# Kernel tuning notes

Measured on AMD Instinct MI355X. Metric: run time of the kernel, lower is better.

The kernel has to match this reference:

```python
import jax, jax.numpy as jnp
import numpy as np

ALPHA = 0.05  # default alpha in __call__
INV_SQRT2 = 0.7071067811865476


def setup_inputs() -> dict:
    key = jax.random.key(0)
    k1, k2 = jax.random.split(key)
    n_objects, n_dim = 16384, 4096
    q_mu = jax.random.normal(k1, (n_objects, n_dim), dtype=jnp.float32)
    # q_var is used as the Normal *scale* in torch.distributions.Normal; keep it positive
    q_var = jax.random.uniform(k2, (n_objects, n_dim), dtype=jnp.float32, minval=0.1, maxval=1.0)
    # buffer built in __init__: arange(1, n+1) / n
    ecdf_factor = jnp.arange(1, n_objects + 1, dtype=jnp.float32) / float(n_objects)
    return {"q_mu": q_mu, "q_var": q_var, "ecdf_factor": ecdf_factor}


def reference(q_mu, q_var, ecdf_factor):
    # pvals[i, j] = Normal(q_mu[i, j], scale=q_var[i, j]).cdf(0)
    pvals = 0.5 * (1.0 + jax.lax.erf((-q_mu / q_var) * INV_SQRT2))  # [n_objects, n_dim]
    pvals = pvals.T  # [n_dim, n_objects] (compute_pvals_torch returns pvals.T)

    # Batched FDR correction (original loops over rows; here fully vectorized).
    sortind = jnp.argsort(pvals, axis=1)                       # [n_dim, n_objects]
    sorted_p = jnp.take_along_axis(pvals, sortind, axis=1)
    reject = sorted_p <= ecdf_factor[None, :] * ALPHA          # bool [n_dim, n_objects]

    # Faithful to the torch code: rejectmax = max(torch.nonzero(reject)[0]) is the
    # FIRST True index (torch.nonzero row 0), then reject[:rejectmax] = True.
    first_idx = jnp.argmax(reject, axis=1)                     # first True (0 if none)
    any_rej = jnp.any(reject, axis=1, keepdims=True)
    col = jnp.arange(reject.shape[1])[None, :]
    reject = jnp.where(any_rej, reject | (col <= first_idx[:, None]), reject)

    # Scatter back to original (unsorted) order: reject_[sortind] = reject
    inv_perm = jnp.argsort(sortind, axis=1)
    reject_unsorted = jnp.take_along_axis(reject, inv_perm, axis=1)

    # fdr tensor is float (empty_like(p_vals)); importance = rejections.sum(dim=1)
    importance = reject_unsorted.astype(pvals.dtype).sum(axis=1)  # [n_dim]
    return importance
```

## Files before the change

kernel.cpp:

```cpp
#include <hip/hip_runtime.h>
#include <math.h>

#define N_OBJ 16384
#define N_DIM 4096
#define BINCAP 4096
#define DPB 16
#define THREADS 1024
#define HWORDS (BINCAP / 2)

__device__ __forceinline__ int bin_fast(float mu, float var) {
    float u = mu * __builtin_amdgcn_rcpf(var);
    float x = u * 0.70710678f;
    bool maybe = (x >= 1.1630f);
    float t = __builtin_amdgcn_rcpf(__builtin_fmaf(0.5f, x, 1.0f));
    float q = 0.17087277f;
    q = __builtin_fmaf(q, t, -0.82215223f);
    q = __builtin_fmaf(q, t, 1.48851587f);
    q = __builtin_fmaf(q, t, -1.13520398f);
    q = __builtin_fmaf(q, t, 0.27886807f);
    q = __builtin_fmaf(q, t, -0.18628806f);
    q = __builtin_fmaf(q, t, 0.09678418f);
    q = __builtin_fmaf(q, t, 0.37409196f);
    q = __builtin_fmaf(q, t, 1.00002368f);
    float ex = __builtin_fmaf(-x, x, -1.26551223f) + t * q;
    float p = maybe ? (0.5f * t * __expf(ex)) : 1.0f;
    bool ok = (p <= 0.05f);
    float pc = fminf(p, 0.0625f);
    int m = (int)(pc * 327680.0f) + 1;
    m = (m > 16384) ? 16384 : m;
    float tm1 = ((float)(m - 1) * (1.0f / 16384.0f)) * 0.05f;
    m -= ((m > 1) && (tm1 >= p)) ? 1 : 0;
    return ok ? (m - 1) : -1;
}

__global__ __launch_bounds__(THREADS) void fused_hist_kernel(
    const float* __restrict__ q_mu, const float* __restrict__ q_var,
    float* __restrict__ out) {
    __shared__ unsigned int hist32[DPB * HWORDS];

    const int tid = threadIdx.x;
    const int b = blockIdx.x;
    const int dimtile = ((b & 7) << 5) | (b >> 3);
    const int d0 = dimtile * DPB;

    for (int i = tid; i < DPB * HWORDS; i += THREADS) hist32[i] = 0u;
    __syncthreads();

    const int dq = (tid & 3) << 2;
    const int orow = tid >> 2;
    size_t base = (size_t)orow * N_DIM + (size_t)(d0 + dq);
    const size_t half = (size_t)256 * N_DIM;
    const size_t step = (size_t)512 * N_DIM;
    unsigned int* __restrict__ h0 = hist32 + dq * HWORDS;

#define ACCUM(mm, ss)                                                          \
    {                                                                          \
        int b0 = bin_fast((mm).x, (ss).x);                                     \
        int b1 = bin_fast((mm).y, (ss).y);                                     \
        int b2 = bin_fast((mm).z, (ss).z);                                     \
        int b3 = bin_fast((mm).w, (ss).w);                                     \
        if ((unsigned)b0 < BINCAP)                                             \
            atomicAdd(&h0[0 * HWORDS + (b0 >> 1)], 1u << ((b0 & 1) << 4));     \
        if ((unsigned)b1 < BINCAP)                                             \
            atomicAdd(&h0[1 * HWORDS + (b1 >> 1)], 1u << ((b1 & 1) << 4));     \
        if ((unsigned)b2 < BINCAP)                                             \
            atomicAdd(&h0[2 * HWORDS + (b2 >> 1)], 1u << ((b2 & 1) << 4));     \
        if ((unsigned)b3 < BINCAP)                                             \
            atomicAdd(&h0[3 * HWORDS + (b3 >> 1)], 1u << ((b3 & 1) << 4));     \
    }

    float4 m0 = *(const float4*)(q_mu + base);
    float4 s0 = *(const float4*)(q_var + base);
    float4 m1 = *(const float4*)(q_mu + base + half);
    float4 s1 = *(const float4*)(q_var + base + half);

    for (int it = 0; it < 31; ++it) {
        const size_t nbase = base + step;
        float4 nm0 = *(const float4*)(q_mu + nbase);
        float4 ns0 = *(const float4*)(q_var + nbase);
        float4 nm1 = *(const float4*)(q_mu + nbase + half);
        float4 ns1 = *(const float4*)(q_var + nbase + half);
        ACCUM(m0, s0);
        ACCUM(m1, s1);
        m0 = nm0; s0 = ns0; m1 = nm1; s1 = ns1;
        base = nbase;
    }
    ACCUM(m0, s0);
    ACCUM(m1, s1);

    __syncthreads();

    const int wave = tid >> 6, lane = tid & 63;
    const unsigned int* H = hist32 + wave * HWORDS;
    unsigned int T = 0;
    unsigned int matches = 0;
    int first = 0x7FFFFFFF;
#pragma unroll 4
    for (int i = 0; i < HWORDS / 64; ++i) {
        unsigned int w = H[i * 64 + lane];
        unsigned int hi = w >> 16;
        unsigned int incl = (w & 0xFFFFu) + hi;
#pragma unroll
        for (int off = 1; off < 64; off <<= 1) {
            unsigned int nbr = __shfl_up(incl, off, 64);
            if (lane >= off) incl += nbr;
        }
        unsigned int run_hi = T + incl;
        unsigned int run_lo = run_hi - hi;
        const int k = (i * 64 + lane) * 2;
        if (run_lo > (unsigned)k) { ++matches; first = min(first, k); }
        if (run_hi > (unsigned)(k + 1)) { ++matches; first = min(first, k + 1); }
        T += __shfl(incl, 63, 64);
    }
#pragma unroll
    for (int off = 32; off >= 1; off >>= 1) {
        matches += __shfl_down(matches, off, 64);
        first = min(first, __shfl_down(first, off, 64));
    }
    if (lane == 0)
        out[d0 + wave] = (first == 0x7FFFFFFF) ? 0.0f : (float)(matches + (unsigned)first);
}

extern "C" void kernel_launch(void* const* d_in, const int* in_sizes, int n_in,
                              void* d_out, int out_size, void* d_ws, size_t ws_size,
                              hipStream_t stream) {
    const float* q_mu = (const float*)d_in[0];
    const float* q_var = (const float*)d_in[1];
    float* out = (float*)d_out;
    (void)d_ws; (void)ws_size;
    fused_hist_kernel<<<dim3(256), dim3(THREADS), 0, stream>>>(q_mu, q_var, out);
}
```

Before: 557.2 us.

## Halve dims per block, double grid, and XOR-swizzle histogram words

Each block now handles 8 dimensions instead of 16, so the grid grows to 512 blocks and shared-memory histograms shrink to 64KB. The intent is more resident blocks per CU and better load balance across CUs. Histogram word indices are also XOR-swizzled per dimension to spread LDS bank conflicts for the atomics. Only 8 of the 16 waves do the scan, and each block reloads the full object range for fewer dims.

Measured after the change: 612.3 us. +9.9%, slower.

```diff
diff --git a/kernel.cpp b/kernel.cpp
--- a/kernel.cpp
+++ b/kernel.cpp
@@ -4,7 +4,7 @@
 #define N_OBJ 16384
 #define N_DIM 4096
 #define BINCAP 4096
-#define DPB 16
+#define DPB 8
 #define THREADS 1024
 #define HWORDS (BINCAP / 2)
 
@@ -33,40 +33,39 @@
     return ok ? (m - 1) : -1;
 }
 
-__global__ __launch_bounds__(THREADS) void fused_hist_kernel(
+__global__ __launch_bounds__(THREADS, 8) void fused_hist_kernel(
     const float* __restrict__ q_mu, const float* __restrict__ q_var,
     float* __restrict__ out) {
     __shared__ unsigned int hist32[DPB * HWORDS];
 
     const int tid = threadIdx.x;
     const int b = blockIdx.x;
-    const int dimtile = ((b & 7) << 5) | (b >> 3);
+    const int dimtile = ((b & 7) << 6) | (b >> 3);
     const int d0 = dimtile * DPB;
 
     for (int i = tid; i < DPB * HWORDS; i += THREADS) hist32[i] = 0u;
     __syncthreads();
 
-    const int dq = (tid & 3) << 2;
-    const int orow = tid >> 2;
+    const int dq = (tid & 1) << 2;
+    const int orow = tid >> 1;
     size_t base = (size_t)orow * N_DIM + (size_t)(d0 + dq);
-    const size_t half = (size_t)256 * N_DIM;
-    const size_t step = (size_t)512 * N_DIM;
+    const size_t half = (size_t)512 * N_DIM;
+    const size_t step = (size_t)1024 * N_DIM;
     unsigned int* __restrict__ h0 = hist32 + dq * HWORDS;
 
-#define ACCUM(mm, ss)                                                          \
-    {                                                                          \
-        int b0 = bin_fast((mm).x, (ss).x);                                     \
-        int b1 = bin_fast((mm).y, (ss).y);                                     \
-        int b2 = bin_fast((mm).z, (ss).z);                                     \
-        int b3 = bin_fast((mm).w, (ss).w);                                     \
-        if ((unsigned)b0 < BINCAP)                                             \
-            atomicAdd(&h0[0 * HWORDS + (b0 >> 1)], 1u << ((b0 & 1) << 4));     \
-        if ((unsigned)b1 < BINCAP)                                             \
-            atomicAdd(&h0[1 * HWORDS + (b1 >> 1)], 1u << ((b1 & 1) << 4));     \
-        if ((unsigned)b2 < BINCAP)                                             \
-            atomicAdd(&h0[2 * HWORDS + (b2 >> 1)], 1u << ((b2 & 1) << 4));     \
-        if ((unsigned)b3 < BINCAP)                                             \
-            atomicAdd(&h0[3 * HWORDS + (b3 >> 1)], 1u << ((b3 & 1) << 4));     \
+#define PUT(bb, ss)                                                              \
+    if ((unsigned)(bb) < BINCAP) {                                               \
+        unsigned int wi = (((unsigned)(bb)) >> 1) ^ (unsigned)(dq + (ss));       \
+        atomicAdd(&h0[(ss) * HWORDS + wi], 1u << (((bb) & 1) << 4));             \
+    }
+
+#define ACCUM(mm, ss_)                                                           \
+    {                                                                            \
+        int b0 = bin_fast((mm).x, (ss_).x);                                      \
+        int b1 = bin_fast((mm).y, (ss_).y);                                      \
+        int b2 = bin_fast((mm).z, (ss_).z);                                      \
+        int b3 = bin_fast((mm).w, (ss_).w);                                      \
+        PUT(b0, 0) PUT(b1, 1) PUT(b2, 2) PUT(b3, 3)                              \
     }
 
     float4 m0 = *(const float4*)(q_mu + base);
@@ -74,7 +73,7 @@
     float4 m1 = *(const float4*)(q_mu + base + half);
     float4 s1 = *(const float4*)(q_var + base + half);
 
-    for (int it = 0; it < 31; ++it) {
+    for (int it = 0; it < 15; ++it) {
         const size_t nbase = base + step;
         float4 nm0 = *(const float4*)(q_mu + nbase);
         float4 ns0 = *(const float4*)(q_var + nbase);
@@ -91,13 +90,15 @@
     __syncthreads();
 
     const int wave = tid >> 6, lane = tid & 63;
+    if (wave >= DPB) return;
     const unsigned int* H = hist32 + wave * HWORDS;
+    const unsigned int xm = (unsigned int)wave;
     unsigned int T = 0;
     unsigned int matches = 0;
     int first = 0x7FFFFFFF;
 #pragma unroll 4
     for (int i = 0; i < HWORDS / 64; ++i) {
-        unsigned int w = H[i * 64 + lane];
+        unsigned int w = H[(unsigned int)(i * 64 + lane) ^ xm];
         unsigned int hi = w >> 16;
         unsigned int incl = (w & 0xFFFFu) + hi;
 #pragma unroll
@@ -128,5 +129,5 @@
     const float* q_var = (const float*)d_in[1];
     float* out = (float*)d_out;
     (void)d_ws; (void)ws_size;
-    fused_hist_kernel<<<dim3(256), dim3(THREADS), 0, stream>>>(q_mu, q_var, out);
+    fused_hist_kernel<<<dim3(512), dim3(THREADS), 0, stream>>>(q_mu, q_var, out);
 }
```
